# Kernel optimization log

Hardware: AMD Instinct MI355X
Metric: run time of the kernel (lower is better)

Reference implementation:

```python
import jax, jax.numpy as jnp
import numpy as np

B, S, H = 2, 1024, 2048
NH, HD = 16, 128
PAST = 1024
ROPE_THETA = 10000.0


def _rope(q, k, theta=ROPE_THETA):
    # q, k: [B, S, NH, HD]; standard rotate-half RoPE over current positions 0..S-1
    s, d = q.shape[1], q.shape[3]
    inv_freq = 1.0 / (theta ** (jnp.arange(0, d, 2, dtype=jnp.float32) / d))  # [d/2]
    freqs = jnp.arange(s, dtype=jnp.float32)[:, None] * inv_freq[None, :]      # [S, d/2]
    emb = jnp.concatenate([freqs, freqs], axis=-1)                             # [S, d]
    cos = jnp.cos(emb)[None, :, None, :]
    sin = jnp.sin(emb)[None, :, None, :]

    def rot_half(x):
        x1, x2 = jnp.split(x, 2, axis=-1)
        return jnp.concatenate([-x2, x1], axis=-1)

    return q * cos + rot_half(q) * sin, k * cos + rot_half(k) * sin


def setup_inputs() -> dict:
    key = jax.random.key(0)
    ks = jax.random.split(key, 12)
    hidden_states = jax.random.normal(ks[0], (B, S, H), dtype=jnp.float32)
    past_key = jax.random.normal(ks[1], (B, NH, PAST, HD), dtype=jnp.float32)
    past_value = jax.random.normal(ks[2], (B, NH, PAST, HD), dtype=jnp.float32)
    # causal mask accounting for cache: 1.0 where masked (query i cannot see kv j > PAST+i)
    q_pos = PAST + jnp.arange(S)[:, None]
    kv_pos = jnp.arange(PAST + S)[None, :]
    mask = jnp.broadcast_to((kv_pos > q_pos).astype(jnp.float32)[None, None], (B, 1, S, PAST + S))
    sc = 1.0 / np.sqrt(H)
    Wq = jax.random.normal(ks[3], (H, NH * HD), dtype=jnp.float32) * sc
    Wk = jax.random.normal(ks[4], (H, NH * HD), dtype=jnp.float32) * sc
    Wv = jax.random.normal(ks[5], (H, NH * HD), dtype=jnp.float32) * sc
    Wo = jax.random.normal(ks[6], (NH * HD, H), dtype=jnp.float32) * (1.0 / np.sqrt(NH * HD))
    bq = jnp.zeros((NH * HD,), jnp.float32)
    bk = jnp.zeros((NH * HD,), jnp.float32)
    bv = jnp.zeros((NH * HD,), jnp.float32)
    bo = jnp.zeros((H,), jnp.float32)
    return {"hidden_states": hidden_states, "mask": mask, "past_key": past_key,
            "past_value": past_value, "Wq": Wq, "bq": bq, "Wk": Wk, "bk": bk,
            "Wv": Wv, "bv": bv, "Wo": Wo, "bo": bo}


def reference(hidden_states, mask, past_key, past_value, Wq, bq, Wk, bk, Wv, bv, Wo, bo):
    b, s, _ = hidden_states.shape
    scale = 1.0 / jnp.sqrt(jnp.float32(HD))
    q = (hidden_states @ Wq + bq).reshape(b, s, NH, HD)
    k = (hidden_states @ Wk + bk).reshape(b, s, NH, HD)
    v = (hidden_states @ Wv + bv).reshape(b, s, NH, HD)
    q, k = _rope(q, k)
    q, k, v = (jnp.transpose(x, (0, 2, 1, 3)) for x in (q, k, v))  # [B,NH,S,HD]
    k = jnp.concatenate([past_key, k], axis=2)    # [B,NH,S_total,HD]
    v = jnp.concatenate([past_value, v], axis=2)
    scores = jnp.einsum('bhqd,bhkd->bhqk', q, k) * scale
    scores = scores + mask * (-1e9)               # mask broadcasts over heads
    probs = jax.nn.softmax(scores, axis=-1).astype(jnp.float32)
    out = jnp.einsum('bhqk,bhkd->bhqd', probs, v)
    out = out.transpose(0, 2, 1, 3).reshape(b, s, NH * HD)
    return out @ Wo + bo, k, v
```

## Files before the change

kernel.cpp:

```cpp
#include <hip/hip_runtime.h>
#include <hip/hip_bf16.h>
#include <math.h>

#define NB 2
#define SEQ 1024
#define HDIM 2048
#define NHEADS 16
#define HDHEAD 128
#define PASTN 1024
#define STOT 2048
#define MROWS 2048

typedef __attribute__((ext_vector_type(4))) float f32x4;
typedef __attribute__((ext_vector_type(8))) __bf16 bf16x8;
typedef __attribute__((ext_vector_type(8))) unsigned short us8;
typedef __attribute__((ext_vector_type(4))) unsigned short us4;

__device__ __forceinline__ unsigned short f2bf(float f) {
    union { float f; unsigned int u; } v; v.f = f;
    unsigned int u = v.u;
    u += 0x7FFFu + ((u >> 16) & 1u);
    return (unsigned short)(u >> 16);
}
__device__ __forceinline__ bf16x8 as_bf(us8 u) { return __builtin_bit_cast(bf16x8, u); }

__device__ __forceinline__ void gl16(const unsigned short* g, unsigned short* l) {
    __builtin_amdgcn_global_load_lds(
        (const __attribute__((address_space(1))) void*)g,
        (__attribute__((address_space(3))) void*)l, 16, 0, 0);
}

#define OFF_CS  ((size_t)0)
#define OFF_HSB (OFF_CS  + (size_t)SEQ*64*8)
#define OFF_WT  (OFF_HSB + (size_t)MROWS*HDIM*2)
#define OFF_QBF (OFF_WT  + (size_t)4*HDIM*HDIM*2)
#define OFF_KC  (OFF_QBF + (size_t)NB*NHEADS*SEQ*HDHEAD*2)
#define OFF_VT  (OFF_KC  + (size_t)NB*NHEADS*STOT*HDHEAD*2)
#define OFF_ATT (OFF_VT  + (size_t)NB*NHEADS*HDHEAD*STOT*2)


__global__ void k_prep1(const float* __restrict__ in, unsigned short* __restrict__ hsb,
                        const float* __restrict__ pk, float* __restrict__ outK,
                        unsigned short* __restrict__ Kc2, float2* __restrict__ csT) {
    const int bid = blockIdx.x, tid = threadIdx.x;
    const int i = (bid * 256 + tid) * 4;
    {
        f32x4 v = *(const f32x4*)(in + i);
        us4 o;
        o.x = f2bf(v.x); o.y = f2bf(v.y); o.z = f2bf(v.z); o.w = f2bf(v.w);
        *(us4*)(hsb + i) = o;
    }
    {
        size_t e = (size_t)i;
        size_t bh = e >> 17;
        int p = (int)((e >> 7) & 1023);
        int d0 = (int)(e & 127);
        f32x4 v = *(const f32x4*)(pk + e);
        __builtin_nontemporal_store(v, (f32x4*)(outK + e + (bh << 17)));
        us4 u;
        u.x = f2bf(v.x); u.y = f2bf(v.y); u.z = f2bf(v.z); u.w = f2bf(v.w);
        const int kt = p >> 6, pr = p & 63;
        *(us4*)(Kc2 + ((bh * 32 + kt) << 13) + (size_t)pr * 128 + (d0 ^ ((p & 7) << 3))) = u;
    }
    if (bid < 256) {
        const int idx = bid * 256 + tid;
        const int s = idx >> 6, fi = idx & 63;
        float inv = 1.0f / powf(10000.0f, (float)fi / 64.0f);
        float a = (float)s * inv;
        csT[idx] = make_float2(cosf(a), sinf(a));
    }
}

__global__ void k_wt(const float* __restrict__ Wq, const float* __restrict__ Wk,
                     const float* __restrict__ Wv, const float* __restrict__ Wo,
                     unsigned short* __restrict__ WT) {
    __shared__ unsigned short t[32][33];
    int z = blockIdx.z;
    const float* W = (z == 0) ? Wq : (z == 1) ? Wk : (z == 2) ? Wv : Wo;
    unsigned short* out = WT + (size_t)z * HDIM * HDIM;
    int n0 = blockIdx.x * 32, k0 = blockIdx.y * 32;
    int tx = threadIdx.x, ty = threadIdx.y;
    #pragma unroll
    for (int j = 0; j < 4; ++j) {
        int kk = ty + j * 8;
        t[kk][tx] = f2bf(W[(size_t)(k0 + kk) * HDIM + n0 + tx]);
    }
    __syncthreads();
    #pragma unroll
    for (int j = 0; j < 4; ++j) {
        int nn = ty + j * 8;
        out[(size_t)(n0 + nn) * HDIM + k0 + tx] = t[tx][nn];
    }
}

__global__ void k_pastv(const float* __restrict__ pv, float* __restrict__ outV,
                        unsigned short* __restrict__ Vt2) {
    __shared__ unsigned short t[64][65];
    int bh = blockIdx.z;
    int p0 = blockIdx.x * 64, d0 = blockIdx.y * 64;
    int tx = threadIdx.x, ty = threadIdx.y;
    const float* src = pv + ((size_t)bh * PASTN + p0) * HDHEAD + d0;
    float* dst = outV + ((size_t)bh * STOT + p0) * HDHEAD + d0;
    #pragma unroll
    for (int j = 0; j < 16; ++j) {
        int pp = ty + j * 4;
        float v = src[(size_t)pp * HDHEAD + tx];
        __builtin_nontemporal_store(v, &dst[(size_t)pp * HDHEAD + tx]);
        t[tx][pp] = f2bf(v);
    }
    __syncthreads();
    unsigned short* vt = Vt2 + (((size_t)bh * 32 + (p0 >> 6)) << 13);
    #pragma unroll
    for (int j = 0; j < 16; ++j) {
        int dd = ty + j * 4;
        const int d = d0 + dd;
        vt[(size_t)d * 64 + (tx ^ ((d & 7) << 3))] = t[dd][tx];
    }
}

__global__ __launch_bounds__(512, 2) void k_gemm_qkv(
    const unsigned short* __restrict__ hsb, const unsigned short* __restrict__ WT,
    const float* __restrict__ bq, const float* __restrict__ bk, const float* __restrict__ bv,
    const float2* __restrict__ csT,
    unsigned short* __restrict__ qbf, unsigned short* __restrict__ Kc2,
    unsigned short* __restrict__ Vt2, float* __restrict__ outK, float* __restrict__ outV) {
    __shared__ __align__(16) unsigned short As[2][256 * 64];
    __shared__ __align__(16) unsigned short Bs[2][256 * 64];

    const int bid = blockIdx.x;
    const int swz = (bid & 7) * 24 + (bid >> 3);
    const int mb = swz & 7;
    const int nbz = swz >> 3;
    const int z = nbz >> 3;
    const int nb8 = nbz & 7;
    const int m0 = mb * 256;
    const int n0 = nb8 * 256;
    const unsigned short* Wz = WT + (size_t)z * HDIM * HDIM;
    const float* bias = (z == 0) ? bq : (z == 1) ? bk : bv;

    const int t = threadIdx.x;
    const int lane = t & 63, wid = t >> 6;
    const int wr = wid >> 1, wc = wid & 1;
    const int c = lane & 15, g = lane >> 4;

    const int lrow8 = lane >> 3;
    const int lslot = (lane & 7) ^ lrow8;
    const unsigned short* aB = hsb + (size_t)(m0 + lrow8) * HDIM + lslot * 8;
    const unsigned short* bB = Wz + (size_t)(n0 + lrow8) * HDIM + lslot * 8;

    auto stage = [&](int kt, int pb) {
        const int k0s = kt * 64;
        #pragma unroll
        for (int j = 0; j < 4; ++j) {
            const int ch = wid * 4 + j;
            gl16(aB + (size_t)(ch * 8) * HDIM + k0s, &As[pb][ch * 512]);
            gl16(bB + (size_t)(ch * 8) * HDIM + k0s, &Bs[pb][ch * 512]);
        }
    };

    f32x4 acc[4][8] = {};
    const int NT = HDIM / 64;

    stage(0, 0);
    stage(1, 1);

    for (int kt = 0; kt < NT; ++kt) {
        const int p = kt & 1;
        if (kt + 1 < NT) {
            asm volatile("s_waitcnt vmcnt(8)" ::: "memory");
        } else {
            asm volatile("s_waitcnt vmcnt(0)" ::: "memory");
        }
        __builtin_amdgcn_s_barrier();
        bf16x8 bfr[8][2];
        #pragma unroll
        for (int ni = 0; ni < 8; ++ni) {
            const int br = wc * 128 + ni * 16 + c;
            const int sw = br & 7;
            bfr[ni][0] = as_bf(*(const us8*)&Bs[p][br * 64 + ((g ^ sw) << 3)]);
            bfr[ni][1] = as_bf(*(const us8*)&Bs[p][br * 64 + (((4 + g) ^ sw) << 3)]);
        }
        #pragma unroll
        for (int mi = 0; mi < 4; ++mi) {
            const int ar = wr * 64 + mi * 16 + c;
            const int swa = ar & 7;
            const bf16x8 a0 = as_bf(*(const us8*)&As[p][ar * 64 + ((g ^ swa) << 3)]);
            const bf16x8 a1 = as_bf(*(const us8*)&As[p][ar * 64 + (((4 + g) ^ swa) << 3)]);
            __builtin_amdgcn_s_setprio(1);
            #pragma unroll
            for (int ni = 0; ni < 8; ++ni)
                acc[mi][ni] = __builtin_amdgcn_mfma_f32_16x16x32_bf16(a0, bfr[ni][0], acc[mi][ni], 0, 0, 0);
            #pragma unroll
            for (int ni = 0; ni < 8; ++ni)
                acc[mi][ni] = __builtin_amdgcn_mfma_f32_16x16x32_bf16(a1, bfr[ni][1], acc[mi][ni], 0, 0, 0);
            __builtin_amdgcn_s_setprio(0);
            __builtin_amdgcn_s_barrier();
        }
        if (kt + 2 < NT) stage(kt + 2, p);
    }

    const float qscale = 0.08838834764831845f * 1.44269504088896f;
    const int h = nb8 * 2 + wc;
    #pragma unroll
    for (int mi = 0; mi < 4; ++mi) {
        #pragma unroll
        for (int r = 0; r < 4; ++r) {
            const int row = m0 + wr * 64 + mi * 16 + g * 4 + r;
            const int b = row >> 10, s = row & 1023;
            const size_t bh2 = (size_t)(b * NHEADS + h);
            const int p = PASTN + s;
            #pragma unroll
            for (int ni = 0; ni < 8; ++ni) {
                const int d = ni * 16 + c;
                const int nglob = n0 + wc * 128 + d;
                const float val = acc[mi][ni][r] + bias[nglob];
                if (z == 2) {
                    __builtin_nontemporal_store(val, &outV[(bh2 * STOT + p) * HDHEAD + d]);
                    Vt2[((bh2 * 32 + (p >> 6)) << 13) + (size_t)d * 64 +
                        ((p & 63) ^ ((d & 7) << 3))] = f2bf(val);
                } else {
                    const int fidx = d & 63;
                    const float2 cs = csT[s * 64 + fidx];
                    const float other = acc[mi][ni ^ 4][r] + bias[nglob ^ 64];
                    const float rot = (d < 64) ? (val * cs.x - other * cs.y)
                                               : (val * cs.x + other * cs.y);
                    if (z == 0) {
                        qbf[(bh2 * SEQ + s) * HDHEAD + d] = f2bf(rot * qscale);
                    } else {
                        Kc2[((bh2 * 32 + (p >> 6)) << 13) + (size_t)(p & 63) * 128 +
                            (d ^ ((p & 7) << 3))] = f2bf(rot);
                        __builtin_nontemporal_store(rot, &outK[(bh2 * STOT + p) * HDHEAD + d]);
                    }
                }
            }
        }
    }
}

__global__ __launch_bounds__(512) void k_attn(
    const unsigned short* __restrict__ qbf, const unsigned short* __restrict__ Kc2,
    const unsigned short* __restrict__ Vt2, unsigned short* __restrict__ attn) {
    __shared__ __align__(16) unsigned short Ks[2][64 * 128];
    __shared__ __align__(16) unsigned short Vs[128 * 64];
    __shared__ __align__(16) unsigned short P[8][16][72];
    const int qt = blockIdx.x;
    const int bh = blockIdx.y;
    const int b = bh >> 4, h = bh & 15;
    const int t = threadIdx.x, lane = t & 63, w = t >> 6;
    const int c = lane & 15, g = lane >> 4;
    const int q0 = qt * 128 + w * 16;
    const unsigned short* Qb = qbf + ((size_t)bh * SEQ + q0) * HDHEAD;
    const unsigned short* Kbase = Kc2 + ((size_t)bh << 18);
    const unsigned short* Vbase = Vt2 + ((size_t)bh << 18);

    bf16x8 qf[4];
    #pragma unroll
    for (int kf = 0; kf < 4; ++kf)
        qf[kf] = as_bf(*(const us8*)(Qb + (size_t)c * HDHEAD + kf * 32 + g * 8));

    #pragma unroll
    for (int j = 0; j < 2; ++j) {
        const int ch = w * 2 + j;
        gl16(Kbase + ch * 512 + lane * 8, &Ks[0][ch * 512]);
    }

    f32x4 o[8] = {};
    float mrow[4] = {-1e30f, -1e30f, -1e30f, -1e30f};
    float lrow[4] = {0.f, 0.f, 0.f, 0.f};
    const int nkt = 18 + 2 * qt;
    int cur = 0;
    for (int kt = 0; kt < nkt; ++kt) {
        asm volatile("s_waitcnt vmcnt(0)" ::: "memory");
        __builtin_amdgcn_s_barrier();
        const unsigned short* Vg = Vbase + ((size_t)kt << 13);
        #pragma unroll
        for (int j = 0; j < 2; ++j) {
            const int ch = w * 2 + j;
            gl16(Vg + ch * 512 + lane * 8, &Vs[ch * 512]);
        }
        if (kt + 1 < nkt) {
            const unsigned short* Kg = Kbase + ((size_t)(kt + 1) << 13);
            #pragma unroll
            for (int j = 0; j < 2; ++j) {
                const int ch = w * 2 + j;
                gl16(Kg + ch * 512 + lane * 8, &Ks[cur ^ 1][ch * 512]);
            }
        }
        f32x4 sa[4] = {};
        #pragma unroll
        for (int nf = 0; nf < 4; ++nf) {
            const int row = nf * 16 + c;
            const int swzr = (row & 7) << 3;
            #pragma unroll
            for (int kf = 0; kf < 4; ++kf) {
                bf16x8 kf8 = as_bf(*(const us8*)&Ks[cur][row * 128 + ((kf * 32 + g * 8) ^ swzr)]);
                sa[nf] = __builtin_amdgcn_mfma_f32_16x16x32_bf16(qf[kf], kf8, sa[nf], 0, 0, 0);
            }
        }
        const int k0 = kt * 64;
        if (k0 + 63 > PASTN + q0) {
            #pragma unroll
            for (int nf = 0; nf < 4; ++nf) {
                const int j = k0 + nf * 16 + c;
                #pragma unroll
                for (int r = 0; r < 4; ++r)
                    if (j > PASTN + q0 + g * 4 + r) sa[nf][r] = -1e30f;
            }
        }
        float pmax[4];
        #pragma unroll
        for (int r = 0; r < 4; ++r)
            pmax[r] = fmaxf(fmaxf(sa[0][r], sa[1][r]), fmaxf(sa[2][r], sa[3][r]));
        bool need = false;
        #pragma unroll
        for (int r = 0; r < 4; ++r) need = need || (pmax[r] > mrow[r] + 12.0f);
        if (__any(need)) {
            #pragma unroll
            for (int r = 0; r < 4; ++r) {
                float mx = pmax[r];
                mx = fmaxf(mx, __shfl_xor(mx, 1));
                mx = fmaxf(mx, __shfl_xor(mx, 2));
                mx = fmaxf(mx, __shfl_xor(mx, 4));
                mx = fmaxf(mx, __shfl_xor(mx, 8));
                const float mnew = fmaxf(mrow[r], mx);
                const float alpha = exp2f(mrow[r] - mnew);
                mrow[r] = mnew;
                lrow[r] *= alpha;
                #pragma unroll
                for (int nd = 0; nd < 8; ++nd) o[nd][r] *= alpha;
            }
        }
        #pragma unroll
        for (int r = 0; r < 4; ++r) {
            const float p0 = exp2f(sa[0][r] - mrow[r]);
            const float p1 = exp2f(sa[1][r] - mrow[r]);
            const float p2 = exp2f(sa[2][r] - mrow[r]);
            const float p3 = exp2f(sa[3][r] - mrow[r]);
            lrow[r] += (p0 + p1) + (p2 + p3);
            P[w][g * 4 + r][0 * 16 + c] = f2bf(p0);
            P[w][g * 4 + r][1 * 16 + c] = f2bf(p1);
            P[w][g * 4 + r][2 * 16 + c] = f2bf(p2);
            P[w][g * 4 + r][3 * 16 + c] = f2bf(p3);
        }
        if (kt + 1 < nkt) {
            asm volatile("s_waitcnt vmcnt(2)" ::: "memory");
        } else {
            asm volatile("s_waitcnt vmcnt(0)" ::: "memory");
        }
        __builtin_amdgcn_s_barrier();
        #pragma unroll
        for (int kf2 = 0; kf2 < 2; ++kf2) {
            const bf16x8 pa = as_bf(*(const us8*)&P[w][c][kf2 * 32 + g * 8]);
            #pragma unroll
            for (int nd = 0; nd < 8; ++nd) {
                const int d = nd * 16 + c;
                const bf16x8 vf = as_bf(*(const us8*)&Vs[d * 64 + ((kf2 * 32 + g * 8) ^ ((d & 7) << 3))]);
                o[nd] = __builtin_amdgcn_mfma_f32_16x16x32_bf16(pa, vf, o[nd], 0, 0, 0);
            }
        }
        cur ^= 1;
    }
    #pragma unroll
    for (int r = 0; r < 4; ++r) {
        float ls = lrow[r];
        ls += __shfl_xor(ls, 1);
        ls += __shfl_xor(ls, 2);
        ls += __shfl_xor(ls, 4);
        ls += __shfl_xor(ls, 8);
        const float inv = 1.0f / ls;
        #pragma unroll
        for (int nd = 0; nd < 8; ++nd) o[nd][r] *= inv;
    }
    #pragma unroll
    for (int nd = 0; nd < 8; ++nd)
        #pragma unroll
        for (int r = 0; r < 4; ++r) {
            const int srow = q0 + g * 4 + r;
            attn[((size_t)b * SEQ + srow) * HDIM + h * HDHEAD + nd * 16 + c] = f2bf(o[nd][r]);
        }
}

__global__ __launch_bounds__(256) void k_gemm_out(
    const unsigned short* __restrict__ attn, const unsigned short* __restrict__ WTo,
    const float* __restrict__ bo, float* __restrict__ out) {
    __shared__ __align__(16) unsigned short As[2][128 * 64];
    __shared__ __align__(16) unsigned short Bs[2][128 * 64];
    const int m0 = blockIdx.y * 128;
    const int n0 = blockIdx.x * 128;
    const int t = threadIdx.x;
    const int lane = t & 63, w = t >> 6;
    const int c = lane & 15, g = lane >> 4;

    const int lrow = lane >> 3;
    const int lslot = (lane & 7) ^ lrow;
    const unsigned short* aB = attn + (size_t)(m0 + lrow) * HDIM + lslot * 8;
    const unsigned short* bB = WTo + (size_t)(n0 + lrow) * HDIM + lslot * 8;

    f32x4 acc[2][8] = {};
    const int NT = HDIM / 64;

    #pragma unroll
    for (int j = 0; j < 4; ++j) {
        const int ch = w * 4 + j;
        gl16(aB + (size_t)(ch * 8) * HDIM, &As[0][ch * 512]);
        gl16(bB + (size_t)(ch * 8) * HDIM, &Bs[0][ch * 512]);
    }
    for (int kt = 0; kt < NT; ++kt) {
        const int cb = kt & 1;
        if (kt + 1 < NT) {
            const int k1 = (kt + 1) * 64;
            #pragma unroll
            for (int j = 0; j < 4; ++j) {
                const int ch = w * 4 + j;
                gl16(aB + (size_t)(ch * 8) * HDIM + k1, &As[cb ^ 1][ch * 512]);
                gl16(bB + (size_t)(ch * 8) * HDIM + k1, &Bs[cb ^ 1][ch * 512]);
            }
            asm volatile("s_waitcnt vmcnt(8)" ::: "memory");
        } else {
            asm volatile("s_waitcnt vmcnt(0)" ::: "memory");
        }
        __builtin_amdgcn_s_barrier();
        #pragma unroll
        for (int kc = 0; kc < 2; ++kc) {
            bf16x8 af[2];
            #pragma unroll
            for (int mi = 0; mi < 2; ++mi) {
                const int ar = w * 32 + mi * 16 + c;
                af[mi] = as_bf(*(const us8*)&As[cb][ar * 64 + (((kc * 4 + g) ^ (ar & 7)) << 3)]);
            }
            #pragma unroll
            for (int ni = 0; ni < 8; ++ni) {
                const int br = ni * 16 + c;
                bf16x8 bfrag = as_bf(*(const us8*)&Bs[cb][br * 64 + (((kc * 4 + g) ^ (br & 7)) << 3)]);
                acc[0][ni] = __builtin_amdgcn_mfma_f32_16x16x32_bf16(af[0], bfrag, acc[0][ni], 0, 0, 0);
                acc[1][ni] = __builtin_amdgcn_mfma_f32_16x16x32_bf16(af[1], bfrag, acc[1][ni], 0, 0, 0);
            }
        }
        __builtin_amdgcn_s_barrier();
    }
    #pragma unroll
    for (int mi = 0; mi < 2; ++mi)
        #pragma unroll
        for (int r = 0; r < 4; ++r) {
            const int row = m0 + w * 32 + mi * 16 + g * 4 + r;
            #pragma unroll
            for (int ni = 0; ni < 8; ++ni) {
                const int f = n0 + ni * 16 + c;
                __builtin_nontemporal_store(acc[mi][ni][r] + bo[f], &out[(size_t)row * HDIM + f]);
            }
        }
}

extern "C" void kernel_launch(void* const* d_in, const int* in_sizes, int n_in,
                              void* d_out, int out_size, void* d_ws, size_t ws_size,
                              hipStream_t stream) {
    const float* hidden = (const float*)d_in[0];
    const float* past_key = (const float*)d_in[2];
    const float* past_value = (const float*)d_in[3];
    const float* Wq = (const float*)d_in[4];
    const float* bq = (const float*)d_in[5];
    const float* Wk = (const float*)d_in[6];
    const float* bk = (const float*)d_in[7];
    const float* Wv = (const float*)d_in[8];
    const float* bv = (const float*)d_in[9];
    const float* Wo = (const float*)d_in[10];
    const float* bo = (const float*)d_in[11];

    float* out0 = (float*)d_out;
    float* outK = out0 + (size_t)NB * SEQ * HDIM;
    float* outV = outK + (size_t)NB * NHEADS * STOT * HDHEAD;

    char* ws = (char*)d_ws;
    float2* csT = (float2*)(ws + OFF_CS);
    unsigned short* hsb = (unsigned short*)(ws + OFF_HSB);
    unsigned short* WT = (unsigned short*)(ws + OFF_WT);
    unsigned short* qbf = (unsigned short*)(ws + OFF_QBF);
    unsigned short* Kc2 = (unsigned short*)(ws + OFF_KC);
    unsigned short* Vt2 = (unsigned short*)(ws + OFF_VT);
    unsigned short* attnb = (unsigned short*)(ws + OFF_ATT);

    k_prep1<<<dim3(4096), dim3(256), 0, stream>>>(hidden, hsb, past_key, outK, Kc2, csT);
    k_wt<<<dim3(64, 64, 4), dim3(32, 8), 0, stream>>>(Wq, Wk, Wv, Wo, WT);
    k_pastv<<<dim3(16, 2, 32), dim3(64, 4), 0, stream>>>(past_value, outV, Vt2);
    k_gemm_qkv<<<dim3(192), dim3(512), 0, stream>>>(
        hsb, WT, bq, bk, bv, csT, qbf, Kc2, Vt2, outK, outV);
    k_attn<<<dim3(8, 32), dim3(512), 0, stream>>>(qbf, Kc2, Vt2, attnb);
    k_gemm_out<<<dim3(16, 16), dim3(256), 0, stream>>>(
        attnb, WT + (size_t)3 * HDIM * HDIM, bo, out0);
}
```

Measured before the change: 239.7 us.

## Stage GEMM epilogues through LDS for vectorized coalesced stores

Both the QKV and output GEMM epilogues now write their accumulator fragments into shared memory, reusing the operand staging buffers, then read them back row-contiguously. This lets each lane issue 16-byte float4 and packed 4×bf16 stores instead of scattered scalar stores. The aim is to cut the cost of uncoalesced global writes for Q, K, V, the transposed V copy and the final output. In exchange it adds barriers and LDS round trips, and drops the QKV kernel's launch bound from 2 to 1 blocks per CU.

Result: slower. 267.1 us (+11.5%).

```diff
diff --git a/kernel.cpp b/kernel.cpp
--- a/kernel.cpp
+++ b/kernel.cpp
@@ -118,14 +118,15 @@
     }
 }
 
-__global__ __launch_bounds__(512, 2) void k_gemm_qkv(
+__global__ __launch_bounds__(512, 1) void k_gemm_qkv(
     const unsigned short* __restrict__ hsb, const unsigned short* __restrict__ WT,
     const float* __restrict__ bq, const float* __restrict__ bk, const float* __restrict__ bv,
     const float2* __restrict__ csT,
     unsigned short* __restrict__ qbf, unsigned short* __restrict__ Kc2,
     unsigned short* __restrict__ Vt2, float* __restrict__ outK, float* __restrict__ outV) {
-    __shared__ __align__(16) unsigned short As[2][256 * 64];
-    __shared__ __align__(16) unsigned short Bs[2][256 * 64];
+    __shared__ __align__(16) unsigned char SMEM[131072];
+    unsigned short* As0 = (unsigned short*)SMEM;
+    unsigned short* Bs0 = (unsigned short*)(SMEM + 65536);
 
     const int bid = blockIdx.x;
     const int swz = (bid & 7) * 24 + (bid >> 3);
@@ -153,8 +154,8 @@
         #pragma unroll
         for (int j = 0; j < 4; ++j) {
             const int ch = wid * 4 + j;
-            gl16(aB + (size_t)(ch * 8) * HDIM + k0s, &As[pb][ch * 512]);
-            gl16(bB + (size_t)(ch * 8) * HDIM + k0s, &Bs[pb][ch * 512]);
+            gl16(aB + (size_t)(ch * 8) * HDIM + k0s, &As0[pb * 16384 + ch * 512]);
+            gl16(bB + (size_t)(ch * 8) * HDIM + k0s, &Bs0[pb * 16384 + ch * 512]);
         }
     };
 
@@ -177,15 +178,15 @@
         for (int ni = 0; ni < 8; ++ni) {
             const int br = wc * 128 + ni * 16 + c;
             const int sw = br & 7;
-            bfr[ni][0] = as_bf(*(const us8*)&Bs[p][br * 64 + ((g ^ sw) << 3)]);
-            bfr[ni][1] = as_bf(*(const us8*)&Bs[p][br * 64 + (((4 + g) ^ sw) << 3)]);
+            bfr[ni][0] = as_bf(*(const us8*)&Bs0[p * 16384 + br * 64 + ((g ^ sw) << 3)]);
+            bfr[ni][1] = as_bf(*(const us8*)&Bs0[p * 16384 + br * 64 + (((4 + g) ^ sw) << 3)]);
         }
         #pragma unroll
         for (int mi = 0; mi < 4; ++mi) {
             const int ar = wr * 64 + mi * 16 + c;
             const int swa = ar & 7;
-            const bf16x8 a0 = as_bf(*(const us8*)&As[p][ar * 64 + ((g ^ swa) << 3)]);
-            const bf16x8 a1 = as_bf(*(const us8*)&As[p][ar * 64 + (((4 + g) ^ swa) << 3)]);
+            const bf16x8 a0 = as_bf(*(const us8*)&As0[p * 16384 + ar * 64 + ((g ^ swa) << 3)]);
+            const bf16x8 a1 = as_bf(*(const us8*)&As0[p * 16384 + ar * 64 + (((4 + g) ^ swa) << 3)]);
             __builtin_amdgcn_s_setprio(1);
             #pragma unroll
             for (int ni = 0; ni < 8; ++ni)
@@ -199,39 +200,75 @@
         if (kt + 2 < NT) stage(kt + 2, p);
     }
 
+    float* myF = (float*)SMEM + wid * (16 * 132);
     const float qscale = 0.08838834764831845f * 1.44269504088896f;
     const int h = nb8 * 2 + wc;
-    #pragma unroll
+    const int b = m0 >> 10;
+    const size_t bh2 = (size_t)(b * NHEADS + h);
+    const int qrow = lane & 31;
+
     for (int mi = 0; mi < 4; ++mi) {
+        __syncthreads();
+        const int s_base = m0 + wr * 64 + mi * 16 - (b << 10);
         #pragma unroll
         for (int r = 0; r < 4; ++r) {
-            const int row = m0 + wr * 64 + mi * 16 + g * 4 + r;
-            const int b = row >> 10, s = row & 1023;
-            const size_t bh2 = (size_t)(b * NHEADS + h);
-            const int p = PASTN + s;
+            const int row = g * 4 + r;
+            const int s = s_base + row;
             #pragma unroll
             for (int ni = 0; ni < 8; ++ni) {
                 const int d = ni * 16 + c;
                 const int nglob = n0 + wc * 128 + d;
                 const float val = acc[mi][ni][r] + bias[nglob];
+                float sv;
                 if (z == 2) {
-                    __builtin_nontemporal_store(val, &outV[(bh2 * STOT + p) * HDHEAD + d]);
-                    Vt2[((bh2 * 32 + (p >> 6)) << 13) + (size_t)d * 64 +
-                        ((p & 63) ^ ((d & 7) << 3))] = f2bf(val);
+                    sv = val;
                 } else {
-                    const int fidx = d & 63;
-                    const float2 cs = csT[s * 64 + fidx];
+                    const float2 cs = csT[s * 64 + (d & 63)];
                     const float other = acc[mi][ni ^ 4][r] + bias[nglob ^ 64];
-                    const float rot = (d < 64) ? (val * cs.x - other * cs.y)
-                                               : (val * cs.x + other * cs.y);
-                    if (z == 0) {
-                        qbf[(bh2 * SEQ + s) * HDHEAD + d] = f2bf(rot * qscale);
-                    } else {
-                        Kc2[((bh2 * 32 + (p >> 6)) << 13) + (size_t)(p & 63) * 128 +
-                            (d ^ ((p & 7) << 3))] = f2bf(rot);
-                        __builtin_nontemporal_store(rot, &outK[(bh2 * STOT + p) * HDHEAD + d]);
-                    }
+                    sv = (d < 64) ? (val * cs.x - other * cs.y)
+                                  : (val * cs.x + other * cs.y);
+                    if (z == 0) sv *= qscale;
                 }
+                myF[row * 132 + d] = sv;
+            }
+        }
+        __syncthreads();
+        #pragma unroll
+        for (int j = 0; j < 8; ++j) {
+            const int rrow = 2 * j + (lane >> 5);
+            const int s = s_base + rrow;
+            const int p = PASTN + s;
+            const f32x4 v4 = *(const f32x4*)&myF[rrow * 132 + qrow * 4];
+            if (z == 0) {
+                us4 u;
+                u.x = f2bf(v4.x); u.y = f2bf(v4.y); u.z = f2bf(v4.z); u.w = f2bf(v4.w);
+                *(us4*)&qbf[(bh2 * SEQ + s) * HDHEAD + qrow * 4] = u;
+            } else if (z == 1) {
+                __builtin_nontemporal_store(v4, (f32x4*)&outK[(bh2 * STOT + p) * HDHEAD + qrow * 4]);
+                us4 u;
+                u.x = f2bf(v4.x); u.y = f2bf(v4.y); u.z = f2bf(v4.z); u.w = f2bf(v4.w);
+                *(us4*)&Kc2[((bh2 * 32 + (p >> 6)) << 13) + (size_t)(p & 63) * 128 +
+                            ((qrow * 4) ^ ((p & 7) << 3))] = u;
+            } else {
+                __builtin_nontemporal_store(v4, (f32x4*)&outV[(bh2 * STOT + p) * HDHEAD + qrow * 4]);
+            }
+        }
+        if (z == 2) {
+            const int p_base = PASTN + s_base;
+            const int ktv = p_base >> 6;
+            const int psub = (lane >> 4) * 4;
+            const int pr0 = (p_base & 63) + psub;
+            unsigned short* vbaseo = Vt2 + ((bh2 * 32 + ktv) << 13);
+            #pragma unroll
+            for (int jj = 0; jj < 8; ++jj) {
+                const int d = jj * 16 + c;
+                const float f0 = myF[(psub + 0) * 132 + d];
+                const float f1 = myF[(psub + 1) * 132 + d];
+                const float f2v = myF[(psub + 2) * 132 + d];
+                const float f3 = myF[(psub + 3) * 132 + d];
+                us4 u;
+                u.x = f2bf(f0); u.y = f2bf(f1); u.z = f2bf(f2v); u.w = f2bf(f3);
+                *(us4*)&vbaseo[d * 64 + (pr0 ^ ((d & 7) << 3))] = u;
             }
         }
     }
@@ -383,8 +420,9 @@
 __global__ __launch_bounds__(256) void k_gemm_out(
     const unsigned short* __restrict__ attn, const unsigned short* __restrict__ WTo,
     const float* __restrict__ bo, float* __restrict__ out) {
-    __shared__ __align__(16) unsigned short As[2][128 * 64];
-    __shared__ __align__(16) unsigned short Bs[2][128 * 64];
+    __shared__ __align__(16) unsigned char SMEM[65536];
+    unsigned short* As0 = (unsigned short*)SMEM;
+    unsigned short* Bs0 = (unsigned short*)(SMEM + 32768);
     const int m0 = blockIdx.y * 128;
     const int n0 = blockIdx.x * 128;
     const int t = threadIdx.x;
@@ -402,8 +440,8 @@
     #pragma unroll
     for (int j = 0; j < 4; ++j) {
         const int ch = w * 4 + j;
-        gl16(aB + (size_t)(ch * 8) * HDIM, &As[0][ch * 512]);
-        gl16(bB + (size_t)(ch * 8) * HDIM, &Bs[0][ch * 512]);
+        gl16(aB + (size_t)(ch * 8) * HDIM, &As0[ch * 512]);
+        gl16(bB + (size_t)(ch * 8) * HDIM, &Bs0[ch * 512]);
     }
     for (int kt = 0; kt < NT; ++kt) {
         const int cb = kt & 1;
@@ -412,8 +450,8 @@
             #pragma unroll
             for (int j = 0; j < 4; ++j) {
                 const int ch = w * 4 + j;
-                gl16(aB + (size_t)(ch * 8) * HDIM + k1, &As[cb ^ 1][ch * 512]);
-                gl16(bB + (size_t)(ch * 8) * HDIM + k1, &Bs[cb ^ 1][ch * 512]);
+                gl16(aB + (size_t)(ch * 8) * HDIM + k1, &As0[(cb ^ 1) * 8192 + ch * 512]);
+                gl16(bB + (size_t)(ch * 8) * HDIM + k1, &Bs0[(cb ^ 1) * 8192 + ch * 512]);
             }
             asm volatile("s_waitcnt vmcnt(8)" ::: "memory");
         } else {
@@ -426,29 +464,41 @@
             #pragma unroll
             for (int mi = 0; mi < 2; ++mi) {
                 const int ar = w * 32 + mi * 16 + c;
-                af[mi] = as_bf(*(const us8*)&As[cb][ar * 64 + (((kc * 4 + g) ^ (ar & 7)) << 3)]);
+                af[mi] = as_bf(*(const us8*)&As0[cb * 8192 + ar * 64 + (((kc * 4 + g) ^ (ar & 7)) << 3)]);
             }
             #pragma unroll
             for (int ni = 0; ni < 8; ++ni) {
                 const int br = ni * 16 + c;
-                bf16x8 bfrag = as_bf(*(const us8*)&Bs[cb][br * 64 + (((kc * 4 + g) ^ (br & 7)) << 3)]);
+                bf16x8 bfrag = as_bf(*(const us8*)&Bs0[cb * 8192 + br * 64 + (((kc * 4 + g) ^ (br & 7)) << 3)]);
                 acc[0][ni] = __builtin_amdgcn_mfma_f32_16x16x32_bf16(af[0], bfrag, acc[0][ni], 0, 0, 0);
                 acc[1][ni] = __builtin_amdgcn_mfma_f32_16x16x32_bf16(af[1], bfrag, acc[1][ni], 0, 0, 0);
             }
         }
         __builtin_amdgcn_s_barrier();
     }
-    #pragma unroll
-    for (int mi = 0; mi < 2; ++mi)
+
+    float* myF = (float*)SMEM + w * (16 * 132);
+    const int qrow = lane & 31;
+    for (int mi = 0; mi < 2; ++mi) {
+        __syncthreads();
         #pragma unroll
         for (int r = 0; r < 4; ++r) {
-            const int row = m0 + w * 32 + mi * 16 + g * 4 + r;
-            #pragma unroll
-            for (int ni = 0; ni < 8; ++ni) {
-                const int f = n0 + ni * 16 + c;
-                __builtin_nontemporal_store(acc[mi][ni][r] + bo[f], &out[(size_t)row * HDIM + f]);
-            }
-        }
+            const int row = g * 4 + r;
+            #pragma unroll
+            for (int ni = 0; ni < 8; ++ni)
+                myF[row * 132 + ni * 16 + c] = acc[mi][ni][r];
+        }
+        __syncthreads();
+        #pragma unroll
+        for (int j = 0; j < 8; ++j) {
+            const int rrow = 2 * j + (lane >> 5);
+            const int row = m0 + w * 32 + mi * 16 + rrow;
+            f32x4 v4 = *(const f32x4*)&myF[rrow * 132 + qrow * 4];
+            const f32x4 b4 = *(const f32x4*)&bo[n0 + qrow * 4];
+            v4 += b4;
+            __builtin_nontemporal_store(v4, (f32x4*)&out[(size_t)row * HDIM + n0 + qrow * 4]);
+        }
+    }
 }
 
 extern "C" void kernel_launch(void* const* d_in, const int* in_sizes, int n_in,
```
